# Kernel optimization log

Hardware: AMD Instinct MI355X
Metric: run time of the kernel (lower is better)

## Reference

```python
import jax, jax.numpy as jnp
import numpy as np
from jax import lax

B, T, D, A, H, C, K = 32, 1500, 512, 512, 4, 10, 100  # batch, frames, key/query/value dim, attn dim, heads, conv channels, conv half-kernel


def setup_inputs() -> dict:
    rng = jax.random.key(0)
    ks = jax.random.split(rng, 13)
    s = 0.02  # param init scale
    return {
        "key": jax.random.normal(ks[0], (B, T, D), jnp.float32),
        "key_lens": jax.random.randint(ks[1], (B,), 3 * T // 4, T + 1, jnp.int32),
        "value": jax.random.normal(ks[2], (B, T, D), jnp.float32),
        "query": jax.random.normal(ks[3], (B, 1, D), jnp.float32),
        "aw": jax.random.uniform(ks[4], (H, B, T), jnp.float32),
        # shared-across-heads linear params (ModuleList([m]*n_heads) shares one module)
        "w_enc_W": jax.random.normal(ks[5], (D, A), jnp.float32) * s,
        "w_enc_b": jnp.zeros((A,), jnp.float32),
        "w_dec_W": jax.random.normal(ks[6], (D, A), jnp.float32) * s,
        "w_conv_W": jax.random.normal(ks[7], (C, A), jnp.float32) * s,
        "v_W": jax.random.normal(ks[8], (A,), jnp.float32) * s,
        # distinct conv kernel per head: grouped-conv layout [H*C, 1, 2K+1]
        "conv_W": jax.random.normal(ks[9], (H * C, 1, 2 * K + 1), jnp.float32) * s,
        "w_out_W": jax.random.normal(ks[10], (D * H, D), jnp.float32) * s,
        "w_out_b": jnp.zeros((D,), jnp.float32),
    }


def reference(key, key_lens, value, query, aw, w_enc_W, w_enc_b, w_dec_W,
              w_conv_W, v_W, conv_W, w_out_W, w_out_b):
    bs, key_len, _ = key.shape
    n_heads = aw.shape[0]
    half_k = (conv_W.shape[-1] - 1) // 2

    # key projection (shared weights => identical key_a for every head): [B,T,A]
    key_a = jnp.einsum('btd,da->bta', key, w_enc_W) + w_enc_b
    # query projection (no bias): [B,1,A]
    dec = jnp.einsum('bqd,da->bqa', query, w_dec_W)

    # location conv feature: distinct kernel per head via grouped 1D conv
    x = jnp.transpose(aw, (1, 0, 2))  # [B,H,T]
    conv_out = lax.conv_general_dilated(
        x, conv_W, window_strides=(1,), padding=[(half_k, half_k)],
        feature_group_count=n_heads,
        dimension_numbers=('NCH', 'OIH', 'NCH'))  # [B,H*C,T]
    conv_feat = jnp.transpose(
        conv_out.reshape(bs, n_heads, -1, key_len), (1, 0, 3, 2))  # [H,B,T,C]
    conv_proj = jnp.einsum('hbtc,ca->hbta', conv_feat, w_conv_W)  # [H,B,T,A]

    # additive score with tanh, reduced by v: [H,B,T]
    e = jnp.einsum('hbta,a->hbt',
                   jnp.tanh(key_a[None] + dec[None] + conv_proj), v_W)

    # length mask + softmax (sharpening_factor=1, no sigmoid smoothing)
    mask = jnp.arange(key_len) < key_lens[:, None]  # [B,T]
    e = jnp.where(mask[None], e, -jnp.inf)
    aw_new = jax.nn.softmax(e, axis=-1)  # [H,B,T]

    # NOTE: source uses the INPUT aw for the context (quirk preserved)
    ctx = jnp.einsum('hbt,btv->bhv', aw, value)  # [B,H,V]
    ctx = ctx.reshape(bs, 1, -1)  # head-major concat, [B,1,H*V]
    out = jnp.einsum('bqk,kd->bqd', ctx, w_out_W) + w_out_b  # [B,1,D]
    return out, aw_new
```

## Files before the change

### kernel.cpp

```cpp
#include <hip/hip_runtime.h>
#include <hip/hip_bf16.h>

#define BB 32
#define TT 1500
#define DD 512
#define AA 512
#define HH 4
#define CC 10
#define KK 100
#define KW 201
#define MM (BB*TT)
#define PS 2.8853900817779268f

typedef unsigned short u16;
typedef unsigned int u32;
typedef __attribute__((ext_vector_type(8))) short bf16x8;
typedef __attribute__((ext_vector_type(4))) float f32x4;
typedef __attribute__((ext_vector_type(4))) unsigned int u32x4;

static __device__ __forceinline__ u16 f2bf(float f) {
    u32 x = __float_as_uint(f);
    return (u16)((x + 0x7fffu + ((x >> 16) & 1u)) >> 16);
}
static __device__ __forceinline__ u32 pkbf(float lo, float hi) {
    u32 r;
    asm("v_cvt_pk_bf16_f32 %0, %1, %2" : "=v"(r) : "v"(lo), "v"(hi));
    return r;
}
static __device__ __forceinline__ void stage16(const void* g, void* l) {
    __builtin_amdgcn_global_load_lds(
        (const __attribute__((address_space(1))) void*)g,
        (__attribute__((address_space(3))) void*)l, 16, 0, 0);
}

__global__ __launch_bounds__(256) void prep_k(
    const float* __restrict__ wencW, const float* __restrict__ q,
    const float* __restrict__ wdec, const float* __restrict__ encb,
    const float* __restrict__ aw, const float* __restrict__ convW,
    u16* __restrict__ wenc_t, float* __restrict__ dec_ps,
    float* __restrict__ cfeat, float* __restrict__ ctx, float* __restrict__ outz)
{
    __shared__ float pls[4160];
    int blk = blockIdx.x, tid = threadIdx.x;
    if (blk < 64) {
        int a0 = (blk & 7) * 64, d0 = (blk >> 3) * 64;
#pragma unroll
        for (int it = 0; it < 16; ++it) {
            int row = it * 4 + (tid >> 6), col = tid & 63;
            pls[row * 65 + col] = wencW[(size_t)(d0 + row) * AA + a0 + col];
        }
        __syncthreads();
#pragma unroll
        for (int it = 0; it < 16; ++it) {
            int ar = it * 4 + (tid >> 6), dc = tid & 63;
            wenc_t[(size_t)(a0 + ar) * DD + d0 + dc] = f2bf(pls[dc * 65 + ar] * PS);
        }
    } else if (blk < 128) {
        int bidx = blk - 64;
        int b = bidx >> 1, a = (bidx & 1) * 256 + tid;
        for (int i = tid; i < DD; i += 256) pls[i] = q[b * DD + i];
        __syncthreads();
        float acc = encb[a];
#pragma unroll 8
        for (int d = 0; d < DD; ++d) acc = fmaf(pls[d], wdec[(size_t)d * AA + a], acc);
        dec_ps[b * AA + a] = acc * PS;
    } else if (blk < 384) {
        int cidx = blk - 128;
        int half = cidx & 1, hb = cidx >> 1;
        int h = hb >> 5, b = hb & 31;
        float* srow = pls;
        float* swk  = pls + 952;
        int tstart = half * 750;
        const float* arow = aw + (size_t)(h * BB + b) * TT;
        for (int i = tid; i < 952; i += 256) {
            int t = tstart + i - KK;
            srow[i] = (t >= 0 && t < TT) ? arow[t] : 0.f;
        }
        for (int i = tid; i < CC * KW; i += 256) swk[i] = convW[h * CC * KW + i];
        __syncthreads();
        if (tid < 250) {
            int tl = tid * 3;
            float acc[CC][3];
#pragma unroll
            for (int c = 0; c < CC; ++c)
#pragma unroll
                for (int u = 0; u < 3; ++u) acc[c][u] = 0.f;
            float r0 = srow[tl], r1 = srow[tl + 1], r2 = srow[tl + 2];
            for (int j = 0; j < KW; ++j) {
#pragma unroll
                for (int c = 0; c < CC; ++c) {
                    float w = swk[c * KW + j];
                    acc[c][0] = fmaf(r0, w, acc[c][0]);
                    acc[c][1] = fmaf(r1, w, acc[c][1]);
                    acc[c][2] = fmaf(r2, w, acc[c][2]);
                }
                r0 = r1; r1 = r2; r2 = srow[tl + j + 3];
            }
            float* dst = cfeat + ((size_t)h * MM + (size_t)b * TT + tstart + tl) * CC;
#pragma unroll
            for (int u = 0; u < 3; ++u)
#pragma unroll
                for (int c = 0; c < CC; ++c) dst[u * CC + c] = acc[c][u];
        }
    } else if (blk < 392) {
        float4* p = (float4*)ctx;
        int bidx = blk - 384;
        float4 z = {0.f, 0.f, 0.f, 0.f};
#pragma unroll
        for (int k2 = 0; k2 < 8; ++k2) p[bidx * 2048 + k2 * 256 + tid] = z;
    } else {
        float4* p = (float4*)outz;
        int bidx = blk - 392;
        float4 z = {0.f, 0.f, 0.f, 0.f};
#pragma unroll
        for (int k2 = 0; k2 < 8; ++k2) p[bidx * 2048 + k2 * 256 + tid] = z;
    }
}

__global__ __launch_bounds__(256) void gemm_e_k(
    const float* __restrict__ key, const u16* __restrict__ Bt,
    const float* __restrict__ dec_ps, const float* __restrict__ cf,
    const float* __restrict__ wconv, const float* __restrict__ vw,
    float* __restrict__ Q4)
{
    __shared__ float smf[5128];
    char* smem = (char*)smf;
    u16* sB = (u16*)(smem + 10240);
    u16* sAe = (u16*)smem;
    u16* sBe = (u16*)(smem + 16384);
    const int ZPAD = 20480;

    int tid = threadIdx.x;
    int orig = blockIdx.x;
    int xcd = orig & 7, idx = orig >> 3;
    int swz = (xcd < 4 ? xcd * 188 : 752 + (xcd - 4) * 187) + idx;
    int bn = swz & 3, bm = swz >> 2;
    int row0 = bm * 128, col0 = bn * 128;
    int lane = tid & 63, wv = tid >> 6;
    int wr = wv >> 1, wc = wv & 1;
    int lhi = lane >> 4, llo = lane & 15;

    f32x4 acc[4][4];
#pragma unroll
    for (int i = 0; i < 4; ++i)
#pragma unroll
        for (int j = 0; j < 4; ++j) acc[i][j] = (f32x4){0.f, 0.f, 0.f, 0.f};

    const float4* gA = (const float4*)(key + (size_t)(row0 + (tid >> 1)) * DD) + (tid & 1) * 4;
    u32 aWoff = (tid >> 1) * 80 + (tid & 1) * 32;
    const u16* gB0 = Bt + (size_t)(col0 + (tid >> 2)) * DD + (tid & 3) * 8;
    u16* lB = sB + tid * 8;

    float4 pa0 = gA[0], pa1 = gA[1], pa2 = gA[2], pa3 = gA[3];
    for (int k0 = 0; k0 < DD; k0 += 32) {
        __syncthreads();
        stage16(gB0 + k0, lB);
        stage16(gB0 + 64 * DD + k0, lB + 2048);
        u32x4 s0, s1;
        s0.x = pkbf(pa0.x, pa0.y); s0.y = pkbf(pa0.z, pa0.w);
        s0.z = pkbf(pa1.x, pa1.y); s0.w = pkbf(pa1.z, pa1.w);
        s1.x = pkbf(pa2.x, pa2.y); s1.y = pkbf(pa2.z, pa2.w);
        s1.z = pkbf(pa3.x, pa3.y); s1.w = pkbf(pa3.z, pa3.w);
        *(u32x4*)(smem + aWoff) = s0;
        *(u32x4*)(smem + aWoff + 16) = s1;
        if (k0 + 32 < DD) {
            int nb = (k0 + 32) >> 2;
            pa0 = gA[nb]; pa1 = gA[nb + 1]; pa2 = gA[nb + 2]; pa3 = gA[nb + 3];
        }
        __syncthreads();

        bf16x8 af[4], bfr[4];
#pragma unroll
        for (int i = 0; i < 4; ++i)
            af[i] = *(const bf16x8*)(smem + (wr * 64 + i * 16 + llo) * 80 + lhi * 16);
#pragma unroll
        for (int j = 0; j < 4; ++j)
            bfr[j] = *(const bf16x8*)(sB + (wc * 64 + j * 16 + llo) * 32 + lhi * 8);
#pragma unroll
        for (int i = 0; i < 4; ++i)
#pragma unroll
            for (int j = 0; j < 4; ++j)
                acc[i][j] = __builtin_amdgcn_mfma_f32_16x16x32_bf16(
                    af[i], bfr[j], acc[i][j], 0, 0, 0);
    }

    __syncthreads();
    int b0 = row0 / TT;
    int boundary = (b0 + 1) * TT - row0;
    int b1 = min(b0 + 1, BB - 1);
    {
        int h = tid >> 6;
#pragma unroll
        for (int e = 0; e < 2; ++e) {
            int r = (tid & 63) * 2 + e;
            const float2* cp = (const float2*)(cf + ((size_t)h * MM + row0 + r) * CC);
            float2 c0 = cp[0], c1 = cp[1], c2 = cp[2], c3 = cp[3], c4 = cp[4];
            u32x4 lo, hi;
            lo.x = pkbf(c0.x, c0.y); lo.y = pkbf(c1.x, c1.y);
            lo.z = pkbf(c2.x, c2.y); lo.w = pkbf(c3.x, c3.y);
            hi.x = pkbf(c4.x, c4.y);
            hi.y = (r < boundary) ? 0x00003f80u : 0x3f800000u;
            hi.z = 0u; hi.w = 0u;
            char* dst = smem + (h * 128 + r) * 32;
            *(u32x4*)dst = lo;
            *(u32x4*)(dst + 16) = hi;
        }
        int col = tid >> 1, kh = tid & 1;
        u32x4 w;
        if (kh == 0) {
            float v0 = wconv[0 * AA + col0 + col] * PS, v1 = wconv[1 * AA + col0 + col] * PS;
            float v2 = wconv[2 * AA + col0 + col] * PS, v3 = wconv[3 * AA + col0 + col] * PS;
            float v4 = wconv[4 * AA + col0 + col] * PS, v5 = wconv[5 * AA + col0 + col] * PS;
            float v6 = wconv[6 * AA + col0 + col] * PS, v7 = wconv[7 * AA + col0 + col] * PS;
            w.x = pkbf(v0, v1); w.y = pkbf(v2, v3); w.z = pkbf(v4, v5); w.w = pkbf(v6, v7);
        } else {
            float v8 = wconv[8 * AA + col0 + col] * PS, v9 = wconv[9 * AA + col0 + col] * PS;
            float d0v = dec_ps[b0 * AA + col0 + col], d1v = dec_ps[b1 * AA + col0 + col];
            w.x = pkbf(v8, v9); w.y = pkbf(d0v, d1v); w.z = 0u; w.w = 0u;
        }
        *(u32x4*)((char*)sBe + col * 32 + kh * 16) = w;
        if (tid == 0) { *(u32x4*)(smem + ZPAD) = (u32x4){0u, 0u, 0u, 0u}; }
    }
    __syncthreads();

    float svj[4];
    bf16x8 be[4];
#pragma unroll
    for (int j = 0; j < 4; ++j) {
        int col = wc * 64 + j * 16 + llo;
        svj[j] = vw[col0 + col];
        u32 off = (lhi < 2) ? (16384u + col * 32 + lhi * 16) : (u32)ZPAD;
        be[j] = *(const bf16x8*)(smem + off);
    }
#pragma unroll
    for (int h = 0; h < 4; ++h) {
#pragma unroll
        for (int i = 0; i < 4; ++i) {
            int rowA = h * 128 + wr * 64 + i * 16 + llo;
            u32 offa = (lhi < 2) ? (rowA * 32 + lhi * 16) : (u32)ZPAD;
            bf16x8 ae = *(const bf16x8*)(smem + offa);
            float ep[4] = {0.f, 0.f, 0.f, 0.f};
#pragma unroll
            for (int j = 0; j < 4; ++j) {
                f32x4 t4 = __builtin_amdgcn_mfma_f32_16x16x32_bf16(ae, be[j], acc[i][j], 0, 0, 0);
#pragma unroll
                for (int r = 0; r < 4; ++r) {
                    float z = exp2f(t4[r]);
                    float p = __builtin_amdgcn_rcpf(1.f + z);
                    ep[r] = fmaf(svj[j], p, ep[r]);
                }
            }
#pragma unroll
            for (int r = 0; r < 4; ++r) {
                float s = ep[r];
                s += __shfl_xor(s, 1);
                s += __shfl_xor(s, 2);
                s += __shfl_xor(s, 4);
                s += __shfl_xor(s, 8);
                if (llo == 0)
                    Q4[((size_t)(bn * HH + h)) * MM + row0 + wr * 64 + i * 16 + lhi * 4 + r] = s;
            }
        }
    }
}

__global__ __launch_bounds__(256) void fin_k(
    const float* __restrict__ Q4, const int* __restrict__ klen,
    const float* __restrict__ aw, const float* __restrict__ value,
    float* __restrict__ aw_new, float* __restrict__ ctx)
{
    __shared__ float fls[1512];
    int blk = blockIdx.x, tid = threadIdx.x;
    if (blk < 128) {
        int h = blk >> 5, b = blk & 31;
        int len = klen[b];
        const float* q0 = Q4 + (size_t)(0 * HH + h) * MM + (size_t)b * TT;
        const float* q1 = Q4 + (size_t)(1 * HH + h) * MM + (size_t)b * TT;
        const float* q2 = Q4 + (size_t)(2 * HH + h) * MM + (size_t)b * TT;
        const float* q3 = Q4 + (size_t)(3 * HH + h) * MM + (size_t)b * TT;
        float* orow = aw_new + (size_t)(h * BB + b) * TT;
        float* rbuf = fls + 1500;
        int lane = tid & 63, wvv = tid >> 6;
        float mx = -3.4e38f;
        for (int t = tid; t < len; t += 256) {
            float e = -2.f * (q0[t] + q1[t] + q2[t] + q3[t]);
            fls[t] = e;
            mx = fmaxf(mx, e);
        }
#pragma unroll
        for (int off = 32; off; off >>= 1) mx = fmaxf(mx, __shfl_xor(mx, off));
        if (lane == 0) rbuf[wvv] = mx;
        __syncthreads();
        mx = fmaxf(fmaxf(rbuf[0], rbuf[1]), fmaxf(rbuf[2], rbuf[3]));
        float sum = 0.f;
        for (int t = tid; t < len; t += 256) {
            float p = __expf(fls[t] - mx);
            fls[t] = p; sum += p;
        }
#pragma unroll
        for (int off = 32; off; off >>= 1) sum += __shfl_xor(sum, off);
        if (lane == 0) rbuf[4 + wvv] = sum;
        __syncthreads();
        float inv = 1.f / (rbuf[4] + rbuf[5] + rbuf[6] + rbuf[7]);
        for (int t = tid; t < TT; t += 256) orow[t] = (t < len) ? fls[t] * inv : 0.f;
    } else {
        int cidx = blk - 128;
        int b = cidx / 25, chunk = cidx - b * 25;
        int c0 = chunk * 60;
        float (*sw)[60] = (float(*)[60])fls;
        if (tid < 240)
            sw[tid / 60][tid % 60] = aw[(size_t)((tid / 60) * BB + b) * TT + c0 + (tid % 60)];
        __syncthreads();
        float a00 = 0, a01 = 0, a10 = 0, a11 = 0, a20 = 0, a21 = 0, a30 = 0, a31 = 0;
        const float* vp = value + ((size_t)b * TT + c0) * DD;
        for (int t = 0; t < 60; ++t) {
            float v0 = vp[(size_t)t * DD + tid];
            float v1 = vp[(size_t)t * DD + tid + 256];
            a00 = fmaf(sw[0][t], v0, a00); a01 = fmaf(sw[0][t], v1, a01);
            a10 = fmaf(sw[1][t], v0, a10); a11 = fmaf(sw[1][t], v1, a11);
            a20 = fmaf(sw[2][t], v0, a20); a21 = fmaf(sw[2][t], v1, a21);
            a30 = fmaf(sw[3][t], v0, a30); a31 = fmaf(sw[3][t], v1, a31);
        }
        atomicAdd(&ctx[(b * HH + 0) * DD + tid], a00);
        atomicAdd(&ctx[(b * HH + 0) * DD + tid + 256], a01);
        atomicAdd(&ctx[(b * HH + 1) * DD + tid], a10);
        atomicAdd(&ctx[(b * HH + 1) * DD + tid + 256], a11);
        atomicAdd(&ctx[(b * HH + 2) * DD + tid], a20);
        atomicAdd(&ctx[(b * HH + 2) * DD + tid + 256], a21);
        atomicAdd(&ctx[(b * HH + 3) * DD + tid], a30);
        atomicAdd(&ctx[(b * HH + 3) * DD + tid + 256], a31);
    }
}

__global__ __launch_bounds__(512) void out_k(const float* __restrict__ ctx,
                                             const float* __restrict__ wout,
                                             const float* __restrict__ wob,
                                             float* __restrict__ out)
{
    int b0 = blockIdx.x * 4, kc = blockIdx.y;
    int tid = threadIdx.x;
    __shared__ float sc[4][64];
    if (tid < 256) sc[tid >> 6][tid & 63] =
        ctx[(size_t)(b0 + (tid >> 6)) * (HH * DD) + kc * 64 + (tid & 63)];
    __syncthreads();
    float acc0 = 0, acc1 = 0, acc2 = 0, acc3 = 0;
    const float* wp = wout + (size_t)(kc * 64) * DD + tid;
#pragma unroll 8
    for (int kk = 0; kk < 64; ++kk) {
        float w = wp[(size_t)kk * DD];
        acc0 = fmaf(sc[0][kk], w, acc0); acc1 = fmaf(sc[1][kk], w, acc1);
        acc2 = fmaf(sc[2][kk], w, acc2); acc3 = fmaf(sc[3][kk], w, acc3);
    }
    if (kc == 0) {
        float bb = wob[tid];
        acc0 += bb; acc1 += bb; acc2 += bb; acc3 += bb;
    }
    atomicAdd(&out[(b0 + 0) * DD + tid], acc0);
    atomicAdd(&out[(b0 + 1) * DD + tid], acc1);
    atomicAdd(&out[(b0 + 2) * DD + tid], acc2);
    atomicAdd(&out[(b0 + 3) * DD + tid], acc3);
}

extern "C" void kernel_launch(void* const* d_in, const int* in_sizes, int n_in,
                              void* d_out, int out_size, void* d_ws, size_t ws_size,
                              hipStream_t stream) {
    const float* key    = (const float*)d_in[0];
    const int*   klen   = (const int*)  d_in[1];
    const float* value  = (const float*)d_in[2];
    const float* query  = (const float*)d_in[3];
    const float* aw     = (const float*)d_in[4];
    const float* wencW  = (const float*)d_in[5];
    const float* wencb  = (const float*)d_in[6];
    const float* wdecW  = (const float*)d_in[7];
    const float* wconvW = (const float*)d_in[8];
    const float* vW     = (const float*)d_in[9];
    const float* convW  = (const float*)d_in[10];
    const float* woutW  = (const float*)d_in[11];
    const float* woutb  = (const float*)d_in[12];

    float* out    = (float*)d_out;
    float* aw_new = out + BB * DD;

    char* ws = (char*)d_ws;
    u16*   wenc_t = (u16*)ws;
    float* dec_ps = (float*)(ws + 524288);
    float* cfeat  = (float*)(ws + 589824);
    float* Q4     = (float*)(ws + 8269824);
    float* ctx    = (float*)(ws + 11341824);

    prep_k  <<<394, 256, 0, stream>>>(wencW, query, wdecW, wencb, aw, convW,
                                      wenc_t, dec_ps, cfeat, ctx, out);
    gemm_e_k<<<1500, 256, 0, stream>>>(key, wenc_t, dec_ps, cfeat, wconvW, vW, Q4);
    fin_k   <<<928, 256, 0, stream>>>(Q4, klen, aw, value, aw_new, ctx);
    out_k   <<<dim3(8, 32), 512, 0, stream>>>(ctx, woutW, woutb, out);
}
```

Baseline: 347.2 us.

## Double-buffer A/B shared tiles in score GEMM with deeper register prefetch

The K-loop of the key-projection GEMM now ping-pongs between two shared-memory buffers for both the bf16-converted key tile and the staged weight tile. This removes one barrier per k-step and lets the global loads and LDS writes for the next step overlap the MFMAs of the current one. The A operand is prefetched two steps ahead in registers. The B tile layout is also changed to a k-chunk-major arrangement, which changes the LDS read pattern. In exchange, LDS use grows to about 36 KB per block and register pressure rises, which may reduce occupancy.

Result: slower. 374.6 us (+7.9%).

```diff
diff --git a/kernel.cpp b/kernel.cpp
--- a/kernel.cpp
+++ b/kernel.cpp
@@ -123,12 +123,8 @@
     const float* __restrict__ wconv, const float* __restrict__ vw,
     float* __restrict__ Q4)
 {
-    __shared__ float smf[5128];
-    char* smem = (char*)smf;
-    u16* sB = (u16*)(smem + 10240);
-    u16* sAe = (u16*)smem;
-    u16* sBe = (u16*)(smem + 16384);
-    const int ZPAD = 20480;
+    __shared__ u32x4 smem4[2305];
+    char* smem = (char*)smem4;
 
     int tid = threadIdx.x;
     int orig = blockIdx.x;
@@ -136,7 +132,8 @@
     int swz = (xcd < 4 ? xcd * 188 : 752 + (xcd - 4) * 187) + idx;
     int bn = swz & 3, bm = swz >> 2;
     int row0 = bm * 128, col0 = bn * 128;
-    int lane = tid & 63, wv = tid >> 6;
+    int lane = tid & 63;
+    int wv = tid >> 6;
     int wr = wv >> 1, wc = wv & 1;
     int lhi = lane >> 4, llo = lane & 15;
 
@@ -148,43 +145,66 @@
 
     const float4* gA = (const float4*)(key + (size_t)(row0 + (tid >> 1)) * DD) + (tid & 1) * 4;
     u32 aWoff = (tid >> 1) * 80 + (tid & 1) * 32;
-    const u16* gB0 = Bt + (size_t)(col0 + (tid >> 2)) * DD + (tid & 3) * 8;
-    u16* lB = sB + tid * 8;
-
-    float4 pa0 = gA[0], pa1 = gA[1], pa2 = gA[2], pa3 = gA[3];
-    for (int k0 = 0; k0 < DD; k0 += 32) {
-        __syncthreads();
-        stage16(gB0 + k0, lB);
-        stage16(gB0 + 64 * DD + k0, lB + 2048);
+    const u16* gBa = Bt + (size_t)(col0 + (tid & 127)) * DD + (tid >> 7) * 8;
+    const u16* gBb = gBa + 16;
+
+    auto loadPA = [&](float4& a0, float4& a1, float4& a2, float4& a3, int s) {
+        a0 = gA[s * 8]; a1 = gA[s * 8 + 1]; a2 = gA[s * 8 + 2]; a3 = gA[s * 8 + 3];
+    };
+    auto stageB = [&](int s, int bbyte) {
+        stage16(gBa + s * 32, (u16*)(smem + bbyte) + (size_t)tid * 8);
+        stage16(gBb + s * 32, (u16*)(smem + bbyte + 4096) + (size_t)tid * 8);
+    };
+    auto writeA = [&](int abyte, float4 q0, float4 q1, float4 q2, float4 q3) {
         u32x4 s0, s1;
-        s0.x = pkbf(pa0.x, pa0.y); s0.y = pkbf(pa0.z, pa0.w);
-        s0.z = pkbf(pa1.x, pa1.y); s0.w = pkbf(pa1.z, pa1.w);
-        s1.x = pkbf(pa2.x, pa2.y); s1.y = pkbf(pa2.z, pa2.w);
-        s1.z = pkbf(pa3.x, pa3.y); s1.w = pkbf(pa3.z, pa3.w);
-        *(u32x4*)(smem + aWoff) = s0;
-        *(u32x4*)(smem + aWoff + 16) = s1;
-        if (k0 + 32 < DD) {
-            int nb = (k0 + 32) >> 2;
-            pa0 = gA[nb]; pa1 = gA[nb + 1]; pa2 = gA[nb + 2]; pa3 = gA[nb + 3];
-        }
-        __syncthreads();
-
+        s0.x = pkbf(q0.x, q0.y); s0.y = pkbf(q0.z, q0.w);
+        s0.z = pkbf(q1.x, q1.y); s0.w = pkbf(q1.z, q1.w);
+        s1.x = pkbf(q2.x, q2.y); s1.y = pkbf(q2.z, q2.w);
+        s1.z = pkbf(q3.x, q3.y); s1.w = pkbf(q3.z, q3.w);
+        *(u32x4*)(smem + abyte + aWoff) = s0;
+        *(u32x4*)(smem + abyte + aWoff + 16) = s1;
+    };
+    auto kstep = [&](int aoff, int boff) {
         bf16x8 af[4], bfr[4];
 #pragma unroll
         for (int i = 0; i < 4; ++i)
-            af[i] = *(const bf16x8*)(smem + (wr * 64 + i * 16 + llo) * 80 + lhi * 16);
+            af[i] = *(const bf16x8*)(smem + aoff + (wr * 64 + i * 16 + llo) * 80 + lhi * 16);
 #pragma unroll
         for (int j = 0; j < 4; ++j)
-            bfr[j] = *(const bf16x8*)(sB + (wc * 64 + j * 16 + llo) * 32 + lhi * 8);
+            bfr[j] = *(const bf16x8*)(smem + boff + (wc * 64 + j * 16 + llo) * 16 + lhi * 2048);
 #pragma unroll
         for (int i = 0; i < 4; ++i)
 #pragma unroll
             for (int j = 0; j < 4; ++j)
                 acc[i][j] = __builtin_amdgcn_mfma_f32_16x16x32_bf16(
                     af[i], bfr[j], acc[i][j], 0, 0, 0);
-    }
-
+    };
+
+    float4 e0, e1, e2, e3, o0, o1, o2, o3;
+    loadPA(e0, e1, e2, e3, 0);
+    stageB(0, 10240);
+    writeA(0, e0, e1, e2, e3);
+    loadPA(o0, o1, o2, o3, 1);
+    loadPA(e0, e1, e2, e3, 2);
     __syncthreads();
+
+#pragma unroll
+    for (int t = 0; t < 16; t += 2) {
+        stageB(t + 1, 28672);
+        writeA(18432, o0, o1, o2, o3);
+        if (t + 3 < 16) loadPA(o0, o1, o2, o3, t + 3);
+        kstep(0, 10240);
+        __syncthreads();
+        if (t + 2 < 16) {
+            stageB(t + 2, 10240);
+            writeA(0, e0, e1, e2, e3);
+            if (t + 4 < 16) loadPA(e0, e1, e2, e3, t + 4);
+        }
+        kstep(18432, 28672);
+        __syncthreads();
+    }
+
+    const int ZPAD = 36864;
     int b0 = row0 / TT;
     int boundary = (b0 + 1) * TT - row0;
     int b1 = min(b0 + 1, BB - 1);
@@ -218,7 +238,7 @@
             float d0v = dec_ps[b0 * AA + col0 + col], d1v = dec_ps[b1 * AA + col0 + col];
             w.x = pkbf(v8, v9); w.y = pkbf(d0v, d1v); w.z = 0u; w.w = 0u;
         }
-        *(u32x4*)((char*)sBe + col * 32 + kh * 16) = w;
+        *(u32x4*)(smem + 16384 + col * 32 + kh * 16) = w;
         if (tid == 0) { *(u32x4*)(smem + ZPAD) = (u32x4){0u, 0u, 0u, 0u}; }
     }
     __syncthreads();
```
